# Performance work log

Hardware: AMD Instinct MI355X
Metric: run time of the kernel (lower is better)

The kernel has to match this reference:

```python
import jax, jax.numpy as jnp
import numpy as np

K = 512
HEADS = 8
B, T, T_CTX = 4, 2048, 2048


def setup_inputs() -> dict:
    key = jax.random.key(0)
    ks = jax.random.split(key, 7)
    scale = 1.0 / np.sqrt(K)
    x = jax.random.normal(ks[0], (B, T, K), dtype=jnp.float32)
    context = jax.random.normal(ks[1], (B, T_CTX, K), dtype=jnp.float32)
    # padding_mask has shape (b*h, t): it is broadcast over the t_context axis
    # of the (b*h, t, t_context) score tensor in the original module.
    padding_mask = jnp.ones((B * HEADS, T), dtype=jnp.int32)
    Wq = jax.random.normal(ks[2], (K, K), dtype=jnp.float32) * scale
    Wk = jax.random.normal(ks[3], (K, K), dtype=jnp.float32) * scale
    Wv = jax.random.normal(ks[4], (K, K), dtype=jnp.float32) * scale
    Wu = jax.random.normal(ks[5], (K, K), dtype=jnp.float32) * scale
    bu = jnp.zeros((K,), dtype=jnp.float32)
    return {"x": x, "context": context, "padding_mask": padding_mask,
            "Wq": Wq, "Wk": Wk, "Wv": Wv, "Wu": Wu, "bu": bu}


def reference(x, context, padding_mask, Wq, Wk, Wv, Wu, bu):
    b, t, e = x.shape
    t_ctx = context.shape[1]
    h = HEADS
    s = e // h
    # Linear projections (torch Linear: x @ W.T)
    q = (x @ Wq.T).reshape(b, t, h, s).transpose(0, 2, 1, 3)          # (b,h,t,s)
    k = (context @ Wk.T).reshape(b, t_ctx, h, s).transpose(0, 2, 1, 3)  # (b,h,c,s)
    v = (context @ Wv.T).reshape(b, t_ctx, h, s).transpose(0, 2, 1, 3)  # (b,h,c,s)
    inv4 = e ** (-0.25)
    dot = jnp.einsum('bhts,bhcs->bhtc', q * inv4, k * inv4)            # (b,h,t,c)
    mask = padding_mask.reshape(b, h, t, 1)
    dot = jnp.where(mask == 0, -jnp.inf, dot)
    att = jax.nn.softmax(dot, axis=-1)
    out = jnp.einsum('bhtc,bhcs->bhts', att, v)                        # (b,h,t,s)
    out = out.transpose(0, 2, 1, 3).reshape(b, t, e)
    return out @ Wu.T + bu
```

## Files before the change

kernel.cpp:

```cpp
#include <hip/hip_runtime.h>
#include <hip/hip_bf16.h>
#include <math.h>


typedef short  s16x8 __attribute__((ext_vector_type(8)));
typedef short  s16x4 __attribute__((ext_vector_type(4)));
typedef float  f32x4 __attribute__((ext_vector_type(4)));
typedef float  f32x8 __attribute__((ext_vector_type(8)));
typedef __bf16 bf16x4v __attribute__((ext_vector_type(4)));
typedef __bf16 bf16x8v __attribute__((ext_vector_type(8)));

#define MFMA_BF16(A, B, C) __builtin_amdgcn_mfma_f32_16x16x32_bf16((A), (B), (C), 0, 0, 0)

__device__ __forceinline__ short f2bf(float f) {
  return (short)__builtin_bit_cast(unsigned short, __float2bfloat16(f));
}

__device__ __forceinline__ void gload_lds16(const void* g, void* l) {
  __builtin_amdgcn_global_load_lds(
      (const __attribute__((address_space(1))) unsigned int*)g,
      (__attribute__((address_space(3))) unsigned int*)l, 16, 0, 0);
}

__global__ void cvt_w(const float* __restrict__ w0, const float* __restrict__ w1,
                      const float* __restrict__ w2, const float* __restrict__ w3,
                      short* __restrict__ o0, short* __restrict__ o1,
                      short* __restrict__ o2, short* __restrict__ o3) {
  int i = blockIdx.x * blockDim.x + threadIdx.x;
  int sel = i >> 16, idx = i & 65535;
  const float* src = sel == 0 ? w0 : sel == 1 ? w1 : sel == 2 ? w2 : w3;
  short*       dst = sel == 0 ? o0 : sel == 1 ? o1 : sel == 2 ? o2 : o3;
  float4 v = ((const float4*)src)[idx];
  s16x4 o;
  o[0] = f2bf(v.x); o[1] = f2bf(v.y); o[2] = f2bf(v.z); o[3] = f2bf(v.w);
  ((s16x4*)dst)[idx] = o;
}

__global__ __launch_bounds__(256, 2)
void proj_qkv(const float* __restrict__ xf, const float* __restrict__ ctxf,
              const short* __restrict__ Wqb, const short* __restrict__ Wkb,
              const short* __restrict__ Wvb,
              short* __restrict__ Qb, short* __restrict__ Kb,
              short* __restrict__ Vtb, float qscale)
{
  __shared__ __align__(16) unsigned char lds[2][24576];
  const int tid  = threadIdx.x;
  const int lane = tid & 63;
  const int w    = tid >> 6;
  const int c0   = lane & 15;
  const int g    = lane >> 4;
  const int bm   = blockIdx.x & 63;
  const int rest = blockIdx.x >> 6;
  const int sel  = rest >> 3;
  const int bn   = rest & 7;
  const int wr   = w >> 1;
  const int wc   = w & 1;

  const float* Af = (sel == 0) ? xf : ctxf;
  const short* Bt = (sel == 0) ? Wqb : (sel == 1) ? Wkb : Wvb;

  const int arow  = tid >> 1;
  const int ahalf = tid & 1;
  const float* abase = Af + (size_t)(bm * 128 + arow) * 512 + ahalf * 32;
  int awoff[4];
  #pragma unroll
  for (int i = 0; i < 4; ++i)
    awoff[i] = arow * 128 + (((ahalf * 4 + i) ^ (arow & 7)) << 4);

  float4 areg[8];
  auto loadA = [&](int kt) {
    const float4* p = (const float4*)(abase + kt * 64);
    #pragma unroll
    for (int i = 0; i < 8; ++i) areg[i] = p[i];
  };
  auto writeA = [&](int buf) {
    #pragma unroll
    for (int i = 0; i < 4; ++i) {
      f32x8 v;
      v[0] = areg[2*i].x; v[1] = areg[2*i].y; v[2] = areg[2*i].z; v[3] = areg[2*i].w;
      v[4] = areg[2*i+1].x; v[5] = areg[2*i+1].y; v[6] = areg[2*i+1].z; v[7] = areg[2*i+1].w;
      *(bf16x8v*)(&lds[buf][awoff[i]]) = __builtin_convertvector(v, bf16x8v);
    }
  };
  auto stageB = [&](int buf, int kt) {
    #pragma unroll
    for (int i = 0; i < 2; ++i) {
      int o   = (i * 256 + tid) << 4;
      int row = o >> 7;
      int sl  = ((o >> 4) & 7) ^ (row & 7);
      gload_lds16(Bt + (size_t)(bn * 64 + row) * 512 + kt * 64 + sl * 8,
                  &lds[buf][16384 + o]);
    }
  };

  f32x4 acc[4][2];
  #pragma unroll
  for (int mi = 0; mi < 4; ++mi)
    #pragma unroll
    for (int ni = 0; ni < 2; ++ni)
      acc[mi][ni] = f32x4{0.f, 0.f, 0.f, 0.f};

  loadA(0);
  stageB(0, 0);
  writeA(0);
  loadA(1);
  __syncthreads();

  for (int kt = 0; kt < 8; ++kt) {
    if (kt < 7) {
      writeA((kt + 1) & 1);
      stageB((kt + 1) & 1, kt + 1);
      if (kt < 6) loadA(kt + 2);
    }
    const unsigned char* lA = lds[kt & 1];
    const unsigned char* lB = lds[kt & 1] + 16384;
    #pragma unroll
    for (int kk = 0; kk < 2; ++kk) {
      s16x8 af[4], bfr[2];
      #pragma unroll
      for (int mi = 0; mi < 4; ++mi) {
        int row  = wr * 64 + mi * 16 + c0;
        int phys = (kk * 4 + g) ^ (row & 7);
        af[mi] = *(const s16x8*)(lA + row * 128 + phys * 16);
      }
      #pragma unroll
      for (int ni = 0; ni < 2; ++ni) {
        int row  = wc * 32 + ni * 16 + c0;
        int phys = (kk * 4 + g) ^ (row & 7);
        bfr[ni] = *(const s16x8*)(lB + row * 128 + phys * 16);
      }
      __builtin_amdgcn_s_setprio(1);
      #pragma unroll
      for (int mi = 0; mi < 4; ++mi)
        #pragma unroll
        for (int ni = 0; ni < 2; ++ni)
          acc[mi][ni] = MFMA_BF16(af[mi], bfr[ni], acc[mi][ni]);
      __builtin_amdgcn_s_setprio(0);
    }
    __syncthreads();
  }

  if (sel == 2) {
    unsigned char* tb = &lds[0][0];
    #pragma unroll
    for (int mi = 0; mi < 4; ++mi) {
      #pragma unroll
      for (int ni = 0; ni < 2; ++ni) {
        int s_l = wc * 32 + ni * 16 + c0;
        int g16 = wr * 8 + mi * 2 + (g >> 1);
        int addr = s_l * 256 + ((g16 ^ (s_l & 7)) << 4) + ((g & 1) << 3);
        f32x4 v = acc[mi][ni];
        bf16x4v pk = __builtin_convertvector(v, bf16x4v);
        *(bf16x4v*)(tb + addr) = pk;
      }
    }
    __syncthreads();
    const int b  = (bm * 128) >> 11;
    const int t0 = (bm * 128) & 2047;
    const int h  = bn;
    #pragma unroll
    for (int it = 0; it < 4; ++it) {
      int s_r = it * 16 + (tid >> 4);
      int tp  = tid & 15;
      s16x8 v = *(const s16x8*)(tb + s_r * 256 + ((tp ^ (s_r & 7)) << 4));
      *(s16x8*)&Vtb[(((size_t)b * 8 + h) * 64 + s_r) * 2048 + t0 + tp * 8] = v;
    }
  } else {
    const float oscale = (sel == 0) ? qscale : 1.0f;
    short* O = (sel == 0) ? Qb : Kb;
    #pragma unroll
    for (int mi = 0; mi < 4; ++mi) {
      #pragma unroll
      for (int ni = 0; ni < 2; ++ni) {
        int row0 = bm * 128 + wr * 64 + mi * 16 + g * 4;
        int col  = bn * 64 + wc * 32 + ni * 16 + c0;
        f32x4 v = acc[mi][ni];
        int h = col >> 6, s = col & 63;
        #pragma unroll
        for (int j = 0; j < 4; ++j) {
          int r = row0 + j;
          int b = r >> 11, t = r & 2047;
          O[(((size_t)b * 8 + h) * 2048 + t) * 64 + s] = f2bf(v[j] * oscale);
        }
      }
    }
  }
}

__global__ __launch_bounds__(256, 2)
void gemm_out(const short* __restrict__ A, const short* __restrict__ Bt,
              const float* __restrict__ bias, float* __restrict__ Cout)
{
  __shared__ __align__(16) unsigned char lds[2][24576];
  const int tid  = threadIdx.x;
  const int lane = tid & 63;
  const int w    = tid >> 6;
  const int c0   = lane & 15;
  const int g    = lane >> 4;
  const int bm   = blockIdx.x & 63;
  const int bn   = blockIdx.x >> 6;
  const int wr   = w >> 1;
  const int wc   = w & 1;

  auto stage = [&](int buf, int kt) {
    #pragma unroll
    for (int i = 0; i < 6; ++i) {
      int o = (i * 256 + tid) << 4;
      if (o < 16384) {
        int row  = o >> 7;
        int ls   = ((o >> 4) & 7) ^ (row & 7);
        gload_lds16(A + (size_t)(bm * 128 + row) * 512 + kt * 64 + ls * 8, &lds[buf][o]);
      } else {
        int o2   = o - 16384;
        int row  = o2 >> 7;
        int ls   = ((o2 >> 4) & 7) ^ (row & 7);
        gload_lds16(Bt + (size_t)(bn * 64 + row) * 512 + kt * 64 + ls * 8, &lds[buf][o]);
      }
    }
  };

  f32x4 acc[4][2];
  #pragma unroll
  for (int mi = 0; mi < 4; ++mi)
    #pragma unroll
    for (int ni = 0; ni < 2; ++ni)
      acc[mi][ni] = f32x4{0.f, 0.f, 0.f, 0.f};

  stage(0, 0);
  for (int kt = 0; kt < 8; ++kt) {
    __syncthreads();
    if (kt < 7) stage((kt + 1) & 1, kt + 1);
    const unsigned char* lA = lds[kt & 1];
    const unsigned char* lB = lds[kt & 1] + 16384;
    #pragma unroll
    for (int kk = 0; kk < 2; ++kk) {
      s16x8 af[4], bfr[2];
      #pragma unroll
      for (int mi = 0; mi < 4; ++mi) {
        int row  = wr * 64 + mi * 16 + c0;
        int phys = (kk * 4 + g) ^ (row & 7);
        af[mi] = *(const s16x8*)(lA + row * 128 + phys * 16);
      }
      #pragma unroll
      for (int ni = 0; ni < 2; ++ni) {
        int row  = wc * 32 + ni * 16 + c0;
        int phys = (kk * 4 + g) ^ (row & 7);
        bfr[ni] = *(const s16x8*)(lB + row * 128 + phys * 16);
      }
      __builtin_amdgcn_s_setprio(1);
      #pragma unroll
      for (int mi = 0; mi < 4; ++mi)
        #pragma unroll
        for (int ni = 0; ni < 2; ++ni)
          acc[mi][ni] = MFMA_BF16(af[mi], bfr[ni], acc[mi][ni]);
      __builtin_amdgcn_s_setprio(0);
    }
  }

  #pragma unroll
  for (int mi = 0; mi < 4; ++mi) {
    #pragma unroll
    for (int ni = 0; ni < 2; ++ni) {
      int row0 = bm * 128 + wr * 64 + mi * 16 + g * 4;
      int col  = bn * 64 + wc * 32 + ni * 16 + c0;
      f32x4 v = acc[mi][ni];
      float bb = bias[col];
      #pragma unroll
      for (int j = 0; j < 4; ++j)
        Cout[(size_t)(row0 + j) * 512 + col] = v[j] + bb;
    }
  }
}

__global__ __launch_bounds__(256, 3)
void attn_fwd(const short* __restrict__ Qb, const short* __restrict__ Kb,
              const short* __restrict__ Vtb, short* __restrict__ Ob)
{
  __shared__ __align__(16) unsigned char sm[49152];

  const int tid  = threadIdx.x;
  const int lane = tid & 63;
  const int w    = tid >> 6;
  const int c0   = lane & 15;
  const int g    = lane >> 4;
  const int bh   = blockIdx.x & 31;
  const int tt   = blockIdx.x >> 5;
  const int c7   = c0 & 7;

  int ka[8];
  #pragma unroll
  for (int kk = 0; kk < 2; ++kk)
    #pragma unroll
    for (int cb = 0; cb < 4; ++cb)
      ka[kk * 4 + cb] = (cb * 16 + c0) * 128 + (((kk * 4 + g) ^ c7) << 4);
  int va[8];
  #pragma unroll
  for (int cm = 0; cm < 2; ++cm)
    #pragma unroll
    for (int sb = 0; sb < 4; ++sb)
      va[cm * 4 + sb] = 8192 + (sb * 16 + c0) * 128 + ((((cm << 2) + g) ^ c7) << 4);
  int pw[2][4], pr[2][2];
  #pragma unroll
  for (int m = 0; m < 2; ++m) {
    int pb = 32768 + w * 4096 + (m * 16 + c0) * 128;
    #pragma unroll
    for (int cb = 0; cb < 4; ++cb)
      pw[m][cb] = pb + ((((2 * cb) + (g >> 1)) ^ c7) << 4) + ((g & 1) << 3);
    #pragma unroll
    for (int cm = 0; cm < 2; ++cm)
      pr[m][cm] = pb + ((((cm << 2) + g) ^ c7) << 4);
  }

  const int to   = tid << 4;
  const int srow = tid >> 3;
  const int sls  = (tid & 7) ^ (srow & 7);
  const int kg0  = srow * 64 + sls * 8;
  const int kg1  = (srow + 32) * 64 + sls * 8;
  const int vg0  = srow * 2048 + sls * 8;
  const int vg1  = (srow + 32) * 2048 + sls * 8;
  int kbase = bh * 131072;
  int vbase = bh * 131072;

  s16x8 qf[2][2];
  const int qrow0 = tt * 128 + w * 32;
  #pragma unroll
  for (int m = 0; m < 2; ++m)
    #pragma unroll
    for (int kk = 0; kk < 2; ++kk)
      qf[m][kk] = *(const s16x8*)(Qb + ((size_t)bh * 2048 + qrow0 + m * 16 + c0) * 64 + kk * 32 + g * 8);

  s16x8 ones;
  #pragma unroll
  for (int i = 0; i < 8; ++i) ones[i] = (short)0x3F80;

  f32x4 accO[4][2];
  #pragma unroll
  for (int sb = 0; sb < 4; ++sb)
    #pragma unroll
    for (int m = 0; m < 2; ++m)
      accO[sb][m] = f32x4{0.f, 0.f, 0.f, 0.f};
  f32x4 lacc[2] = {f32x4{0.f,0.f,0.f,0.f}, f32x4{0.f,0.f,0.f,0.f}};
  float mrow[2] = {-__builtin_inff(), -__builtin_inff()};

  gload_lds16(Kb  + kbase + kg0, sm + to);
  gload_lds16(Kb  + kbase + kg1, sm + 4096 + to);
  gload_lds16(Vtb + vbase + vg0, sm + 8192 + to);
  gload_lds16(Vtb + vbase + vg1, sm + 12288 + to);
  kbase += 4096; vbase += 64;
  __syncthreads();

#define ATTN_TILE(BUF, NOTLAST)                                               \
  {                                                                           \
    if (NOTLAST) {                                                            \
      constexpr int DB = ((BUF) ^ 1) * 16384;                                 \
      gload_lds16(Kb  + kbase + kg0, sm + DB + to);                           \
      gload_lds16(Kb  + kbase + kg1, sm + DB + 4096 + to);                    \
      gload_lds16(Vtb + vbase + vg0, sm + DB + 8192 + to);                    \
      gload_lds16(Vtb + vbase + vg1, sm + DB + 12288 + to);                   \
      kbase += 4096; vbase += 64;                                             \
    }                                                                         \
    constexpr int BO = (BUF) * 16384;                                         \
    f32x4 st[4][2];                                                           \
    _Pragma("unroll")                                                         \
    for (int cb = 0; cb < 4; ++cb) {                                          \
      st[cb][0] = f32x4{0.f, 0.f, 0.f, 0.f};                                  \
      st[cb][1] = f32x4{0.f, 0.f, 0.f, 0.f};                                  \
    }                                                                         \
    __builtin_amdgcn_s_setprio(1);                                            \
    _Pragma("unroll")                                                         \
    for (int kk = 0; kk < 2; ++kk)                                            \
      _Pragma("unroll")                                                       \
      for (int cb = 0; cb < 4; ++cb) {                                        \
        s16x8 kf = *(const s16x8*)(sm + BO + ka[kk * 4 + cb]);                \
        st[cb][0] = MFMA_BF16(kf, qf[0][kk], st[cb][0]);                      \
        st[cb][1] = MFMA_BF16(kf, qf[1][kk], st[cb][1]);                      \
      }                                                                       \
    __builtin_amdgcn_s_setprio(0);                                            \
    float tmax0 = st[0][0][0], tmax1 = st[0][1][0];                           \
    _Pragma("unroll")                                                         \
    for (int cb = 0; cb < 4; ++cb)                                            \
      _Pragma("unroll")                                                       \
      for (int j = 0; j < 4; ++j) {                                           \
        tmax0 = fmaxf(tmax0, st[cb][0][j]);                                   \
        tmax1 = fmaxf(tmax1, st[cb][1][j]);                                   \
      }                                                                       \
    float need = fmaxf(tmax0 - mrow[0], tmax1 - mrow[1]);                     \
    if (__any(need > 8.f)) {                                                  \
      float tm0 = fmaxf(tmax0, __shfl_xor(tmax0, 16));                        \
      tm0 = fmaxf(tm0, __shfl_xor(tm0, 32));                                  \
      float tm1 = fmaxf(tmax1, __shfl_xor(tmax1, 16));                        \
      tm1 = fmaxf(tm1, __shfl_xor(tm1, 32));                                  \
      float mn0 = fmaxf(mrow[0], tm0), mn1 = fmaxf(mrow[1], tm1);             \
      float a0 = __builtin_amdgcn_exp2f(mrow[0] - mn0);                       \
      float a1 = __builtin_amdgcn_exp2f(mrow[1] - mn1);                       \
      mrow[0] = mn0; mrow[1] = mn1;                                           \
      _Pragma("unroll")                                                       \
      for (int j = 0; j < 4; ++j) { lacc[0][j] *= a0; lacc[1][j] *= a1; }     \
      _Pragma("unroll")                                                       \
      for (int sb = 0; sb < 4; ++sb)                                          \
        _Pragma("unroll")                                                     \
        for (int j = 0; j < 4; ++j) {                                         \
          accO[sb][0][j] *= a0;                                               \
          accO[sb][1][j] *= a1;                                               \
        }                                                                     \
    }                                                                         \
    _Pragma("unroll")                                                         \
    for (int m = 0; m < 2; ++m)                                               \
      _Pragma("unroll")                                                       \
      for (int cb = 0; cb < 4; ++cb) {                                        \
        f32x4 p;                                                              \
        _Pragma("unroll")                                                     \
        for (int j = 0; j < 4; ++j)                                           \
          p[j] = __builtin_amdgcn_exp2f(st[cb][m][j] - mrow[m]);              \
        bf16x4v pk = __builtin_convertvector(p, bf16x4v);                     \
        *(bf16x4v*)(sm + pw[m][cb]) = pk;                                     \
      }                                                                       \
    __builtin_amdgcn_s_setprio(1);                                            \
    _Pragma("unroll")                                                         \
    for (int cm = 0; cm < 2; ++cm) {                                          \
      s16x8 pf0 = *(const s16x8*)(sm + pr[0][cm]);                            \
      s16x8 pf1 = *(const s16x8*)(sm + pr[1][cm]);                            \
      lacc[0] = MFMA_BF16(ones, pf0, lacc[0]);                                \
      lacc[1] = MFMA_BF16(ones, pf1, lacc[1]);                                \
      _Pragma("unroll")                                                       \
      for (int sb = 0; sb < 4; ++sb) {                                        \
        s16x8 vf = *(const s16x8*)(sm + BO + va[cm * 4 + sb]);                \
        accO[sb][0] = MFMA_BF16(vf, pf0, accO[sb][0]);                        \
        accO[sb][1] = MFMA_BF16(vf, pf1, accO[sb][1]);                        \
      }                                                                       \
    }                                                                         \
    __builtin_amdgcn_s_setprio(0);                                            \
    __syncthreads();                                                          \
  }

  for (int it = 0; it < 16; ++it) {
    ATTN_TILE(0, true);
    ATTN_TILE(1, (it < 15));
  }
#undef ATTN_TILE

  const int b = bh >> 3, h = bh & 7;
  #pragma unroll
  for (int m = 0; m < 2; ++m) {
    const float inv = 1.0f / lacc[m][0];
    const int t_glob = qrow0 + m * 16 + c0;
    #pragma unroll
    for (int sb = 0; sb < 4; ++sb) {
      f32x4 o4;
      #pragma unroll
      for (int j = 0; j < 4; ++j) o4[j] = accO[sb][m][j] * inv;
      bf16x4v pk = __builtin_convertvector(o4, bf16x4v);
      int s = sb * 16 + g * 4;
      *(bf16x4v*)&Ob[(((size_t)b * 2048 + t_glob) * 8 + h) * 64 + s] = pk;
    }
  }
}

extern "C" void kernel_launch(void* const* d_in, const int* in_sizes, int n_in,
                              void* d_out, int out_size, void* d_ws, size_t ws_size,
                              hipStream_t stream) {
  const float* x       = (const float*)d_in[0];
  const float* context = (const float*)d_in[1];
  const float* Wq = (const float*)d_in[3];
  const float* Wk = (const float*)d_in[4];
  const float* Wv = (const float*)d_in[5];
  const float* Wu = (const float*)d_in[6];
  const float* bu = (const float*)d_in[7];

  char* ws = (char*)d_ws;
  const size_t MB = 1ull << 20;
  short* Qb   = (short*)(ws);
  short* Kb   = (short*)(ws + 8 * MB);
  short* Vtb  = (short*)(ws + 16 * MB);
  short* Ob   = (short*)(ws + 24 * MB);
  short* Wqb  = (short*)(ws + 32 * MB);
  short* Wkb  = (short*)(ws + 32 * MB + 512 * 1024);
  short* Wvb  = (short*)(ws + 33 * MB);
  short* Wub  = (short*)(ws + 33 * MB + 512 * 1024);

  const float SM_SCALE_LOG2E = 0.044194173824159216f * 1.4426950408889634f;

  cvt_w<<<1024, 256, 0, stream>>>(Wq, Wk, Wv, Wu, Wqb, Wkb, Wvb, Wub);
  proj_qkv<<<1536, 256, 0, stream>>>(x, context, Wqb, Wkb, Wvb,
                                     Qb, Kb, Vtb, SM_SCALE_LOG2E);
  attn_fwd<<<512, 256, 0, stream>>>(Qb, Kb, Vtb, Ob);
  gemm_out<<<512, 256, 0, stream>>>(Ob, Wub, bu, (float*)d_out);
}
```

Measured before the change: 198.7 us.

## Pre-convert activations to bf16 and stage both GEMM operands via direct LDS loads

A separate pass now converts x and context to bf16 in workspace, next to the weights. The QKV projection then stages both A and B tiles with global_load_lds instead of loading fp32 into registers and converting in-kernel. The V-transpose epilogue goes straight to global with 4-element strided stores rather than through LDS, and the loop sync is moved to the top of each iteration. The trade is an extra full read and write of the activations in the convert kernel, plus less coalesced Vt stores, in exchange for fewer registers and a simpler pipeline.

```diff
diff --git a/kernel.cpp b/kernel.cpp
--- a/kernel.cpp
+++ b/kernel.cpp
@@ -6,9 +6,7 @@
 typedef short  s16x8 __attribute__((ext_vector_type(8)));
 typedef short  s16x4 __attribute__((ext_vector_type(4)));
 typedef float  f32x4 __attribute__((ext_vector_type(4)));
-typedef float  f32x8 __attribute__((ext_vector_type(8)));
 typedef __bf16 bf16x4v __attribute__((ext_vector_type(4)));
-typedef __bf16 bf16x8v __attribute__((ext_vector_type(8)));
 
 #define MFMA_BF16(A, B, C) __builtin_amdgcn_mfma_f32_16x16x32_bf16((A), (B), (C), 0, 0, 0)
 
@@ -22,14 +20,22 @@
       (__attribute__((address_space(3))) unsigned int*)l, 16, 0, 0);
 }
 
-__global__ void cvt_w(const float* __restrict__ w0, const float* __restrict__ w1,
-                      const float* __restrict__ w2, const float* __restrict__ w3,
-                      short* __restrict__ o0, short* __restrict__ o1,
-                      short* __restrict__ o2, short* __restrict__ o3) {
+__global__ void cvt_all(const float* __restrict__ x, const float* __restrict__ ctx,
+                        const float* __restrict__ w0, const float* __restrict__ w1,
+                        const float* __restrict__ w2, const float* __restrict__ w3,
+                        short* __restrict__ ox, short* __restrict__ octx,
+                        short* __restrict__ o0, short* __restrict__ o1,
+                        short* __restrict__ o2, short* __restrict__ o3) {
   int i = blockIdx.x * blockDim.x + threadIdx.x;
-  int sel = i >> 16, idx = i & 65535;
-  const float* src = sel == 0 ? w0 : sel == 1 ? w1 : sel == 2 ? w2 : w3;
-  short*       dst = sel == 0 ? o0 : sel == 1 ? o1 : sel == 2 ? o2 : o3;
+  const float* src; short* dst; int idx;
+  if (i < 1048576)      { src = x;   dst = ox;   idx = i; }
+  else if (i < 2097152) { src = ctx; dst = octx; idx = i - 1048576; }
+  else {
+    int j = i - 2097152;
+    int sel = j >> 16; idx = j & 65535;
+    src = sel == 0 ? w0 : sel == 1 ? w1 : sel == 2 ? w2 : w3;
+    dst = sel == 0 ? o0 : sel == 1 ? o1 : sel == 2 ? o2 : o3;
+  }
   float4 v = ((const float4*)src)[idx];
   s16x4 o;
   o[0] = f2bf(v.x); o[1] = f2bf(v.y); o[2] = f2bf(v.z); o[3] = f2bf(v.w);
@@ -37,59 +43,42 @@
 }
 
 __global__ __launch_bounds__(256, 2)
-void proj_qkv(const float* __restrict__ xf, const float* __restrict__ ctxf,
+void proj_qkv(const short* __restrict__ xb, const short* __restrict__ ctxb,
               const short* __restrict__ Wqb, const short* __restrict__ Wkb,
               const short* __restrict__ Wvb,
               short* __restrict__ Qb, short* __restrict__ Kb,
               short* __restrict__ Vtb, float qscale)
 {
   __shared__ __align__(16) unsigned char lds[2][24576];
-  const int tid  = threadIdx.x;
-  const int lane = tid & 63;
-  const int w    = tid >> 6;
-  const int c0   = lane & 15;
-  const int g    = lane >> 4;
-  const int bm   = blockIdx.x & 63;
-  const int rest = blockIdx.x >> 6;
-  const int sel  = rest >> 3;
-  const int bn   = rest & 7;
-  const int wr   = w >> 1;
-  const int wc   = w & 1;
-
-  const float* Af = (sel == 0) ? xf : ctxf;
+  const int tid   = threadIdx.x;
+  const int lane  = tid & 63;
+  const int w     = tid >> 6;
+  const int c0    = lane & 15;
+  const int g     = lane >> 4;
+  const int bm    = blockIdx.x & 63;
+  const int rest  = blockIdx.x >> 6;
+  const int sel   = rest >> 3;
+  const int bn    = rest & 7;
+  const int wr    = w >> 1;
+  const int wc    = w & 1;
+
+  const short* A  = (sel == 0) ? xb : ctxb;
   const short* Bt = (sel == 0) ? Wqb : (sel == 1) ? Wkb : Wvb;
 
-  const int arow  = tid >> 1;
-  const int ahalf = tid & 1;
-  const float* abase = Af + (size_t)(bm * 128 + arow) * 512 + ahalf * 32;
-  int awoff[4];
-  #pragma unroll
-  for (int i = 0; i < 4; ++i)
-    awoff[i] = arow * 128 + (((ahalf * 4 + i) ^ (arow & 7)) << 4);
-
-  float4 areg[8];
-  auto loadA = [&](int kt) {
-    const float4* p = (const float4*)(abase + kt * 64);
-    #pragma unroll
-    for (int i = 0; i < 8; ++i) areg[i] = p[i];
-  };
-  auto writeA = [&](int buf) {
-    #pragma unroll
-    for (int i = 0; i < 4; ++i) {
-      f32x8 v;
-      v[0] = areg[2*i].x; v[1] = areg[2*i].y; v[2] = areg[2*i].z; v[3] = areg[2*i].w;
-      v[4] = areg[2*i+1].x; v[5] = areg[2*i+1].y; v[6] = areg[2*i+1].z; v[7] = areg[2*i+1].w;
-      *(bf16x8v*)(&lds[buf][awoff[i]]) = __builtin_convertvector(v, bf16x8v);
-    }
-  };
-  auto stageB = [&](int buf, int kt) {
-    #pragma unroll
-    for (int i = 0; i < 2; ++i) {
-      int o   = (i * 256 + tid) << 4;
-      int row = o >> 7;
-      int sl  = ((o >> 4) & 7) ^ (row & 7);
-      gload_lds16(Bt + (size_t)(bn * 64 + row) * 512 + kt * 64 + sl * 8,
-                  &lds[buf][16384 + o]);
+  auto stage = [&](int buf, int kt) {
+    #pragma unroll
+    for (int i = 0; i < 6; ++i) {
+      int o = (i * 256 + tid) << 4;
+      if (o < 16384) {
+        int row  = o >> 7;
+        int ls   = ((o >> 4) & 7) ^ (row & 7);
+        gload_lds16(A + (size_t)(bm * 128 + row) * 512 + kt * 64 + ls * 8, &lds[buf][o]);
+      } else {
+        int o2   = o - 16384;
+        int row  = o2 >> 7;
+        int ls   = ((o2 >> 4) & 7) ^ (row & 7);
+        gload_lds16(Bt + (size_t)(bn * 64 + row) * 512 + kt * 64 + ls * 8, &lds[buf][o]);
+      }
     }
   };
 
@@ -100,18 +89,10 @@
     for (int ni = 0; ni < 2; ++ni)
       acc[mi][ni] = f32x4{0.f, 0.f, 0.f, 0.f};
 
-  loadA(0);
-  stageB(0, 0);
-  writeA(0);
-  loadA(1);
-  __syncthreads();
-
+  stage(0, 0);
   for (int kt = 0; kt < 8; ++kt) {
-    if (kt < 7) {
-      writeA((kt + 1) & 1);
-      stageB((kt + 1) & 1, kt + 1);
-      if (kt < 6) loadA(kt + 2);
-    }
+    __syncthreads();
+    if (kt < 7) stage((kt + 1) & 1, kt + 1);
     const unsigned char* lA = lds[kt & 1];
     const unsigned char* lB = lds[kt & 1] + 16384;
     #pragma unroll
@@ -137,51 +118,31 @@
           acc[mi][ni] = MFMA_BF16(af[mi], bfr[ni], acc[mi][ni]);
       __builtin_amdgcn_s_setprio(0);
     }
-    __syncthreads();
-  }
-
-  if (sel == 2) {
-    unsigned char* tb = &lds[0][0];
-    #pragma unroll
-    for (int mi = 0; mi < 4; ++mi) {
-      #pragma unroll
-      for (int ni = 0; ni < 2; ++ni) {
-        int s_l = wc * 32 + ni * 16 + c0;
-        int g16 = wr * 8 + mi * 2 + (g >> 1);
-        int addr = s_l * 256 + ((g16 ^ (s_l & 7)) << 4) + ((g & 1) << 3);
-        f32x4 v = acc[mi][ni];
-        bf16x4v pk = __builtin_convertvector(v, bf16x4v);
-        *(bf16x4v*)(tb + addr) = pk;
-      }
-    }
-    __syncthreads();
-    const int b  = (bm * 128) >> 11;
-    const int t0 = (bm * 128) & 2047;
-    const int h  = bn;
-    #pragma unroll
-    for (int it = 0; it < 4; ++it) {
-      int s_r = it * 16 + (tid >> 4);
-      int tp  = tid & 15;
-      s16x8 v = *(const s16x8*)(tb + s_r * 256 + ((tp ^ (s_r & 7)) << 4));
-      *(s16x8*)&Vtb[(((size_t)b * 8 + h) * 64 + s_r) * 2048 + t0 + tp * 8] = v;
-    }
-  } else {
-    const float oscale = (sel == 0) ? qscale : 1.0f;
-    short* O = (sel == 0) ? Qb : Kb;
-    #pragma unroll
-    for (int mi = 0; mi < 4; ++mi) {
-      #pragma unroll
-      for (int ni = 0; ni < 2; ++ni) {
-        int row0 = bm * 128 + wr * 64 + mi * 16 + g * 4;
-        int col  = bn * 64 + wc * 32 + ni * 16 + c0;
-        f32x4 v = acc[mi][ni];
-        int h = col >> 6, s = col & 63;
+  }
+
+  const float oscale = (sel == 0) ? qscale : 1.0f;
+  #pragma unroll
+  for (int mi = 0; mi < 4; ++mi) {
+    #pragma unroll
+    for (int ni = 0; ni < 2; ++ni) {
+      int row0 = bm * 128 + wr * 64 + mi * 16 + g * 4;
+      int col  = bn * 64 + wc * 32 + ni * 16 + c0;
+      f32x4 v = acc[mi][ni];
+      int h = col >> 6, s = col & 63;
+      if (sel < 2) {
+        short* O = (sel == 0) ? Qb : Kb;
         #pragma unroll
         for (int j = 0; j < 4; ++j) {
           int r = row0 + j;
           int b = r >> 11, t = r & 2047;
           O[(((size_t)b * 8 + h) * 2048 + t) * 64 + s] = f2bf(v[j] * oscale);
         }
+      } else {
+        int b = row0 >> 11, t0 = row0 & 2047;
+        s16x4 pk;
+        #pragma unroll
+        for (int j = 0; j < 4; ++j) pk[j] = f2bf(v[j]);
+        *(s16x4*)&Vtb[(((size_t)b * 8 + h) * 64 + s) * 2048 + t0] = pk;
       }
     }
   }
@@ -469,19 +430,22 @@
 
   char* ws = (char*)d_ws;
   const size_t MB = 1ull << 20;
-  short* Qb   = (short*)(ws);
-  short* Kb   = (short*)(ws + 8 * MB);
-  short* Vtb  = (short*)(ws + 16 * MB);
-  short* Ob   = (short*)(ws + 24 * MB);
-  short* Wqb  = (short*)(ws + 32 * MB);
-  short* Wkb  = (short*)(ws + 32 * MB + 512 * 1024);
-  short* Wvb  = (short*)(ws + 33 * MB);
-  short* Wub  = (short*)(ws + 33 * MB + 512 * 1024);
+  short* xb   = (short*)(ws);
+  short* ctxb = (short*)(ws + 8 * MB);
+  short* Qb   = (short*)(ws + 16 * MB);
+  short* Kb   = (short*)(ws + 24 * MB);
+  short* Vtb  = (short*)(ws + 32 * MB);
+  short* Ob   = xb;
+  short* Wqb  = (short*)(ws + 40 * MB);
+  short* Wkb  = (short*)(ws + 40 * MB + 512 * 1024);
+  short* Wvb  = (short*)(ws + 41 * MB);
+  short* Wub  = (short*)(ws + 41 * MB + 512 * 1024);
 
   const float SM_SCALE_LOG2E = 0.044194173824159216f * 1.4426950408889634f;
 
-  cvt_w<<<1024, 256, 0, stream>>>(Wq, Wk, Wv, Wu, Wqb, Wkb, Wvb, Wub);
-  proj_qkv<<<1536, 256, 0, stream>>>(x, context, Wqb, Wkb, Wvb,
+  cvt_all<<<9216, 256, 0, stream>>>(x, context, Wq, Wk, Wv, Wu,
+                                    xb, ctxb, Wqb, Wkb, Wvb, Wub);
+  proj_qkv<<<1536, 256, 0, stream>>>(xb, ctxb, Wqb, Wkb, Wvb,
                                      Qb, Kb, Vtb, SM_SCALE_LOG2E);
   attn_fwd<<<512, 256, 0, stream>>>(Qb, Kb, Vtb, Ob);
   gemm_out<<<512, 256, 0, stream>>>(Ob, Wub, bu, (float*)d_out);
```

Result: faster. 170.3 us (-14.3%).
